# Performance work log

Measured on AMD Instinct MI355X. Metric: run time of the kernel, lower is better.

Reference implementation:

```python
import jax, jax.numpy as jnp
import numpy as np

B, L, K, E, D, H = 16, 512, 48, 128, 384, 128

def _gelu(x):
    return jax.nn.gelu(x, approximate=False)  # torch nn.GELU default is erf-based

def setup_inputs() -> dict:
    key = jax.random.key(0)
    ks = jax.random.split(key, 16)
    def randn(k, shape, scale=1.0):
        return jax.random.normal(k, shape, dtype=jnp.float32) * scale
    inp = {
        "h_V": randn(ks[0], (B, L, D)),
        "h_E": randn(ks[1], (B, L, K, E)),
        "mask": jnp.ones((B, L), dtype=jnp.float32),
        "fw1": randn(ks[2], (E, D), 1.0 / np.sqrt(E)),
        "fb1": randn(ks[3], (D,), 0.02),
        "fw2": randn(ks[4], (D, D), 1.0 / np.sqrt(D)),
        "fb2": randn(ks[5], (D,), 0.02),
        "hw1": randn(ks[6], (D, H), 1.0 / np.sqrt(D)),
        "hb1": randn(ks[7], (H,), 0.02),
        "hw2": randn(ks[8], (H, H // 2), 1.0 / np.sqrt(H)),
        "hb2": randn(ks[9], (H // 2,), 0.02),
        "hw3": randn(ks[10], (H // 2, 1), 1.0 / np.sqrt(H // 2)),
        "hb3": randn(ks[11], (1,), 0.02),
        "E_idx": jax.random.randint(ks[12], (B, L, K), 0, L),
    }
    return inp

def reference(h_V, h_E, mask, fw1, fb1, fw2, fb2, hw1, hb1, hw2, hb2, hw3, hb3, E_idx):
    # CFConv: edge-conditioned filters [B,L,K,D]
    W = _gelu(_gelu(h_E @ fw1 + fb1) @ fw2 + fb2)
    # gather_nodes: x_j[b,l,k,:] = h_V[b, E_idx[b,l,k], :]
    x_j = jax.vmap(lambda x, idx: x[idx])(h_V, E_idx)  # [B,L,K,D]
    h = jnp.sum(x_j * W, axis=2)  # weighted sum over neighbors -> [B,L,D]
    # mlp_head (dropout = identity at inference)
    h = _gelu(h @ hw1 + hb1)
    h = _gelu(h @ hw2 + hb2)
    dG = (h @ hw3 + hb3)[..., 0]  # [B,L]
    valid_length = jnp.clip(jnp.sum(mask, axis=1), 1.0, None)  # [B]
    return jnp.sum(dG * mask, axis=1) / jnp.sqrt(valid_length)  # [B]
```

## Files before the change

kernel.cpp:

```cpp
#include <hip/hip_runtime.h>
#include <hip/hip_bf16.h>
#include <math.h>

#define NB 16
#define NL 512
#define NK 48
#define NE 128
#define ND 384
#define NH 128

typedef __attribute__((ext_vector_type(8))) short short8;
typedef __attribute__((ext_vector_type(4))) float f32x4;

__device__ __forceinline__ float gelu_fast(float x) {
    float t = x * fmaf(x * x, -0.1029437f, -2.3022087f);
    float e = __builtin_amdgcn_exp2f(t);
    return x * __builtin_amdgcn_rcpf(1.0f + e);
}

__device__ __forceinline__ unsigned short f2bf(float x) {
    union { float f; unsigned u; } v; v.f = x;
    unsigned r = v.u + 0x7fffu + ((v.u >> 16) & 1u);
    return (unsigned short)(r >> 16);
}

__device__ __forceinline__ unsigned short f2bf_rhu(float x) {
    union { float f; unsigned u; } v; v.f = x;
    return (unsigned short)((v.u + 0x8000u) >> 16);
}

__device__ __forceinline__ unsigned pk_bf16(float a, float b) {
    union { float f; unsigned u; } ua, ub; ua.f = a; ub.f = b;
    return __builtin_amdgcn_perm(ua.u + 0x8000u, ub.u + 0x8000u, 0x07060302u);
}

__global__ void pack_weights(const float* __restrict__ fw1,
                             const float* __restrict__ fw2,
                             const float* __restrict__ hw1,
                             const float* __restrict__ hw2,
                             unsigned short* __restrict__ fw1p,
                             unsigned short* __restrict__ fw2p,
                             unsigned short* __restrict__ hw1p,
                             unsigned short* __restrict__ hw2p) {
    int tid = blockIdx.x * 256 + threadIdx.x;
    if (tid < NE * ND) {
        int k = tid / ND, n = tid % ND;
        int dst = (((k >> 5) * 24 + (n >> 4)) * 64 + ((k >> 3) & 3) * 16 + (n & 15)) * 8 + (k & 7);
        fw1p[dst] = f2bf(fw1[tid]);
    } else if (tid < NE * ND + ND * ND) {
        int i = tid - NE * ND;
        int k = i / ND, n = i % ND;
        int dst = (((k >> 5) * 24 + (n >> 4)) * 64 + ((k >> 3) & 3) * 16 + (n & 15)) * 8 + (k & 7);
        fw2p[dst] = f2bf(fw2[i]);
    } else if (tid < NE * ND + ND * ND + ND * NH) {
        int i = tid - (NE * ND + ND * ND);
        int k = i / NH, n = i % NH;
        int dst = (((k >> 5) * 8 + (n >> 4)) * 64 + ((k >> 3) & 3) * 16 + (n & 15)) * 8 + (k & 7);
        hw1p[dst] = f2bf(hw1[i]);
    } else if (tid < NE * ND + ND * ND + ND * NH + NH * (NH / 2)) {
        int i = tid - (NE * ND + ND * ND + ND * NH);
        int k = i / (NH / 2), n = i % (NH / 2);
        int dst = (((k >> 5) * 4 + (n >> 4)) * 64 + ((k >> 3) & 3) * 16 + (n & 15)) * 8 + (k & 7);
        hw2p[dst] = f2bf(hw2[i]);
    }
}

__global__ __launch_bounds__(256, 3) void cfconv_kernel(
    const float* __restrict__ h_V, const float* __restrict__ h_E,
    const float* __restrict__ fb1, const float* __restrict__ fb2,
    const unsigned short* __restrict__ fw1p,
    const unsigned short* __restrict__ fw2p,
    const int* __restrict__ E_idx, unsigned short* __restrict__ hbufB)
{
    __shared__ unsigned short Ea[48 * 136];
    __shared__ unsigned short T[48 * 392];
    __shared__ int rowoff_s[48];

    const int t = threadIdx.x;
    const int wave = t >> 6, lane = t & 63;
    const int quad = lane >> 4, l16 = lane & 15;
    const int bl = blockIdx.x;
    const int wn0 = wave * 96;

    if (t < 48)
        rowoff_s[t] = ((bl >> 9) * NL + E_idx[bl * NK + t]) * ND;

    {
        const float4* src = (const float4*)(h_E + (size_t)bl * (NK * NE));
        #pragma unroll
        for (int i = 0; i < 6; i++) {
            int v = i * 256 + t;
            float4 d = src[v];
            int r = v >> 5;
            int c = (v & 31) * 4;
            uint2 u;
            u.x = pk_bf16(d.y, d.x);
            u.y = pk_bf16(d.w, d.z);
            *(uint2*)&Ea[r * 136 + c] = u;
        }
    }
    __syncthreads();

    f32x4 acc[18];

    #pragma unroll
    for (int i = 0; i < 18; i++) acc[i] = (f32x4){0.f, 0.f, 0.f, 0.f};

    #pragma unroll
    for (int kt = 0; kt < 4; kt++) {
        short8 aw[6], be[3];
        #pragma unroll
        for (int mt = 0; mt < 6; mt++)
            aw[mt] = *(const short8*)(fw1p + (size_t)((kt * 24 + (wn0 >> 4) + mt) * 64 + lane) * 8);
        #pragma unroll
        for (int nt = 0; nt < 3; nt++)
            be[nt] = *(const short8*)&Ea[(nt * 16 + l16) * 136 + kt * 32 + quad * 8];
        #pragma unroll
        for (int mt = 0; mt < 6; mt++)
            #pragma unroll
            for (int nt = 0; nt < 3; nt++)
                acc[mt * 3 + nt] = __builtin_amdgcn_mfma_f32_16x16x32_bf16(
                    aw[mt], be[nt], acc[mt * 3 + nt], 0, 0, 0);
    }

    #pragma unroll
    for (int mt = 0; mt < 6; mt++) {
        float4 b1v = *(const float4*)&fb1[wn0 + mt * 16 + quad * 4];
        #pragma unroll
        for (int nt = 0; nt < 3; nt++) {
            f32x4 a = acc[mt * 3 + nt];
            float v0 = gelu_fast(a[0] + b1v.x);
            float v1 = gelu_fast(a[1] + b1v.y);
            float v2 = gelu_fast(a[2] + b1v.z);
            float v3 = gelu_fast(a[3] + b1v.w);
            uint2 u;
            u.x = pk_bf16(v1, v0);
            u.y = pk_bf16(v3, v2);
            *(uint2*)&T[(nt * 16 + l16) * 392 + wn0 + mt * 16 + quad * 4] = u;
        }
    }
    __syncthreads();

    #pragma unroll
    for (int i = 0; i < 18; i++) acc[i] = (f32x4){0.f, 0.f, 0.f, 0.f};

    {
        short8 b0[6], b1[6], af[3];
        #define LOADB(kt, bf)                                                            \
            _Pragma("unroll")                                                            \
            for (int nt = 0; nt < 6; nt++)                                               \
                bf[nt] = *(const short8*)(fw2p +                                         \
                    (size_t)(((kt) * 24 + (wn0 >> 4) + nt) * 64 + lane) * 8);
        #define LOADA(kt)                                                                \
            _Pragma("unroll")                                                            \
            for (int mt = 0; mt < 3; mt++)                                               \
                af[mt] = *(const short8*)&T[(mt * 16 + l16) * 392 + (kt) * 32 + quad * 8];
        #define MFMAS(bf)                                                                \
            _Pragma("unroll")                                                            \
            for (int mt = 0; mt < 3; mt++)                                               \
                _Pragma("unroll")                                                        \
                for (int nt = 0; nt < 6; nt++)                                           \
                    acc[nt * 3 + mt] = __builtin_amdgcn_mfma_f32_16x16x32_bf16(          \
                        af[mt], bf[nt], acc[nt * 3 + mt], 0, 0, 0);

        LOADB(0, b0);
        for (int kt = 0; kt < 10; kt += 2) {
            LOADB(kt + 1, b1);
            LOADA(kt);
            MFMAS(b0);
            LOADB(kt + 2, b0);
            LOADA(kt + 1);
            MFMAS(b1);
        }
        LOADB(11, b1);
        LOADA(10);
        MFMAS(b0);
        LOADA(11);
        MFMAS(b1);
        #undef LOADB
        #undef LOADA
        #undef MFMAS
    }

    float b2v[6];
    #pragma unroll
    for (int nt = 0; nt < 6; nt++) b2v[nt] = fb2[wn0 + nt * 16 + l16];

    float s[6] = {0.f, 0.f, 0.f, 0.f, 0.f, 0.f};
    #pragma unroll
    for (int mt = 0; mt < 3; mt++) {
        const int rb = mt * 16 + quad * 4;
        const float* p0 = h_V + rowoff_s[rb + 0] + wn0 + l16;
        const float* p1 = h_V + rowoff_s[rb + 1] + wn0 + l16;
        const float* p2 = h_V + rowoff_s[rb + 2] + wn0 + l16;
        const float* p3 = h_V + rowoff_s[rb + 3] + wn0 + l16;
        float xv[6][4];
        #pragma unroll
        for (int nt = 0; nt < 6; nt++) {
            xv[nt][0] = p0[nt * 16];
            xv[nt][1] = p1[nt * 16];
            xv[nt][2] = p2[nt * 16];
            xv[nt][3] = p3[nt * 16];
        }
        #pragma unroll
        for (int nt = 0; nt < 6; nt++)
            #pragma unroll
            for (int r = 0; r < 4; r++)
                s[nt] = fmaf(gelu_fast(acc[nt * 3 + mt][r] + b2v[nt]), xv[nt][r], s[nt]);
    }
    #pragma unroll
    for (int nt = 0; nt < 6; nt++) {
        float v = s[nt];
        v += __shfl_xor(v, 16, 64);
        v += __shfl_xor(v, 32, 64);
        if (lane < 16)
            hbufB[(size_t)bl * ND + wn0 + nt * 16 + lane] = f2bf(v);
    }
}

__global__ __launch_bounds__(64) void head_kernel(
    const unsigned short* __restrict__ hbufB,
    const unsigned short* __restrict__ hw1p, const float* __restrict__ hb1,
    const unsigned short* __restrict__ hw2p, const float* __restrict__ hb2,
    const float* __restrict__ hw3, const float* __restrict__ hb3,
    const float* __restrict__ mask, float* __restrict__ dGpart)
{
    __shared__ unsigned short T1[16 * 136];
    const int lane = threadIdx.x;
    const int quad = lane >> 4, l16 = lane & 15;
    const int row0 = blockIdx.x * 16;

    f32x4 acc1[8];
    #pragma unroll
    for (int nt = 0; nt < 8; nt++) acc1[nt] = (f32x4){0.f, 0.f, 0.f, 0.f};

    for (int kt = 0; kt < 12; kt++) {
        short8 a = *(const short8*)(hbufB + (size_t)(row0 + l16) * ND + kt * 32 + quad * 8);
        #pragma unroll
        for (int nt = 0; nt < 8; nt++) {
            short8 b = *(const short8*)(hw1p + (size_t)((kt * 8 + nt) * 64 + lane) * 8);
            acc1[nt] = __builtin_amdgcn_mfma_f32_16x16x32_bf16(a, b, acc1[nt], 0, 0, 0);
        }
    }

    #pragma unroll
    for (int nt = 0; nt < 8; nt++) {
        int col = nt * 16 + l16;
        float b1 = hb1[col];
        #pragma unroll
        for (int r = 0; r < 4; r++)
            T1[(quad * 4 + r) * 136 + col] = f2bf_rhu(gelu_fast(acc1[nt][r] + b1));
    }
    __syncthreads();

    f32x4 acc2[4];
    #pragma unroll
    for (int nt = 0; nt < 4; nt++) acc2[nt] = (f32x4){0.f, 0.f, 0.f, 0.f};

    #pragma unroll
    for (int kt = 0; kt < 4; kt++) {
        short8 a = *(const short8*)&T1[l16 * 136 + kt * 32 + quad * 8];
        #pragma unroll
        for (int nt = 0; nt < 4; nt++) {
            short8 b = *(const short8*)(hw2p + (size_t)((kt * 4 + nt) * 64 + lane) * 8);
            acc2[nt] = __builtin_amdgcn_mfma_f32_16x16x32_bf16(a, b, acc2[nt], 0, 0, 0);
        }
    }

    float w3[4], b2[4];
    #pragma unroll
    for (int nt = 0; nt < 4; nt++) { w3[nt] = hw3[nt * 16 + l16]; b2[nt] = hb2[nt * 16 + l16]; }

    float dsum = 0.f;
    const float hb3v = hb3[0];
    #pragma unroll
    for (int r = 0; r < 4; r++) {
        float pr = 0.f;
        #pragma unroll
        for (int nt = 0; nt < 4; nt++)
            pr = fmaf(gelu_fast(acc2[nt][r] + b2[nt]), w3[nt], pr);
        pr += __shfl_xor(pr, 1, 64);
        pr += __shfl_xor(pr, 2, 64);
        pr += __shfl_xor(pr, 4, 64);
        pr += __shfl_xor(pr, 8, 64);
        if (l16 == 0) {
            int grow = row0 + quad * 4 + r;
            dsum = fmaf(pr + hb3v, mask[grow], dsum);
        }
    }
    dsum += __shfl_xor(dsum, 16, 64);
    dsum += __shfl_xor(dsum, 32, 64);
    if (lane == 0) dGpart[blockIdx.x] = dsum;
}

__global__ void finalize_kernel(const float* __restrict__ dGpart,
                                const float* __restrict__ mask,
                                float* __restrict__ out) {
    int t = threadIdx.x;
    int b = t >> 4, j = t & 15;
    float ms = 0.f;
    for (int l = j; l < NL; l += 16) ms += mask[b * NL + l];
    float dg = dGpart[b * 32 + j] + dGpart[b * 32 + 16 + j];
    #pragma unroll
    for (int d = 1; d < 16; d <<= 1) {
        ms += __shfl_xor(ms, d, 64);
        dg += __shfl_xor(dg, d, 64);
    }
    if (j == 0) {
        ms = fmaxf(ms, 1.0f);
        out[b] = dg / sqrtf(ms);
    }
}

extern "C" void kernel_launch(void* const* d_in, const int* in_sizes, int n_in,
                              void* d_out, int out_size, void* d_ws, size_t ws_size,
                              hipStream_t stream) {
    const float* h_V  = (const float*)d_in[0];
    const float* h_E  = (const float*)d_in[1];
    const float* mask = (const float*)d_in[2];
    const float* fw1  = (const float*)d_in[3];
    const float* fb1  = (const float*)d_in[4];
    const float* fw2  = (const float*)d_in[5];
    const float* fb2  = (const float*)d_in[6];
    const float* hw1  = (const float*)d_in[7];
    const float* hb1  = (const float*)d_in[8];
    const float* hw2  = (const float*)d_in[9];
    const float* hb2  = (const float*)d_in[10];
    const float* hw3  = (const float*)d_in[11];
    const float* hb3  = (const float*)d_in[12];
    const int*   E_idx = (const int*)d_in[13];
    float* out = (float*)d_out;

    char* ws = (char*)d_ws;
    unsigned short* fw1p = (unsigned short*)ws;
    unsigned short* fw2p = (unsigned short*)(ws + 98304);
    unsigned short* hw1p = (unsigned short*)(ws + 393216);
    unsigned short* hw2p = (unsigned short*)(ws + 491520);
    float* dGpart = (float*)(ws + 507904);
    unsigned short* hbufB = (unsigned short*)(ws + 512000);

    pack_weights<<<992, 256, 0, stream>>>(fw1, fw2, hw1, hw2, fw1p, fw2p, hw1p, hw2p);
    cfconv_kernel<<<NB * NL, 256, 0, stream>>>(h_V, h_E, fb1, fb2, fw1p, fw2p, E_idx, hbufB);
    head_kernel<<<(NB * NL) / 16, 64, 0, stream>>>(hbufB, hw1p, hb1, hw2p, hb2, hw3, hb3, mask, dGpart);
    finalize_kernel<<<1, 256, 0, stream>>>(dGpart, mask, out);
}
```

Measured before the change: 466.9 us.

## Alias cfconv LDS buffers, raise occupancy, split head across two waves, vectorize packing

The cfconv kernel now shares one LDS buffer between the edge-feature tile and the intermediate filter tile, with an extra barrier before the overwrite. Launch bounds are raised to target four blocks per CU, which cuts LDS per block to allow more resident blocks. The head kernel splits its output columns across two waves and writes twice as many partials, and finalize sums four partials per row. Weight packing writes 8 bf16 values per thread as one vector store. The tighter occupancy target may force register spills in the main kernel.

```diff
diff --git a/kernel.cpp b/kernel.cpp
--- a/kernel.cpp
+++ b/kernel.cpp
@@ -43,38 +43,33 @@
                              unsigned short* __restrict__ hw1p,
                              unsigned short* __restrict__ hw2p) {
     int tid = blockIdx.x * 256 + threadIdx.x;
-    if (tid < NE * ND) {
-        int k = tid / ND, n = tid % ND;
-        int dst = (((k >> 5) * 24 + (n >> 4)) * 64 + ((k >> 3) & 3) * 16 + (n & 15)) * 8 + (k & 7);
-        fw1p[dst] = f2bf(fw1[tid]);
-    } else if (tid < NE * ND + ND * ND) {
-        int i = tid - NE * ND;
-        int k = i / ND, n = i % ND;
-        int dst = (((k >> 5) * 24 + (n >> 4)) * 64 + ((k >> 3) & 3) * 16 + (n & 15)) * 8 + (k & 7);
-        fw2p[dst] = f2bf(fw2[i]);
-    } else if (tid < NE * ND + ND * ND + ND * NH) {
-        int i = tid - (NE * ND + ND * ND);
-        int k = i / NH, n = i % NH;
-        int dst = (((k >> 5) * 8 + (n >> 4)) * 64 + ((k >> 3) & 3) * 16 + (n & 15)) * 8 + (k & 7);
-        hw1p[dst] = f2bf(hw1[i]);
-    } else if (tid < NE * ND + ND * ND + ND * NH + NH * (NH / 2)) {
-        int i = tid - (NE * ND + ND * ND + ND * NH);
-        int k = i / (NH / 2), n = i % (NH / 2);
-        int dst = (((k >> 5) * 4 + (n >> 4)) * 64 + ((k >> 3) & 3) * 16 + (n & 15)) * 8 + (k & 7);
-        hw2p[dst] = f2bf(hw2[i]);
-    }
-}
-
-__global__ __launch_bounds__(256, 3) void cfconv_kernel(
+    const float* src; unsigned short* dst; int N, NT, idx;
+    if (tid < 6144)        { src = fw1; dst = fw1p; N = ND;     NT = 24; idx = tid; }
+    else if (tid < 24576)  { src = fw2; dst = fw2p; N = ND;     NT = 24; idx = tid - 6144; }
+    else if (tid < 30720)  { src = hw1; dst = hw1p; N = NH;     NT = 8;  idx = tid - 24576; }
+    else                   { src = hw2; dst = hw2p; N = NH / 2; NT = 4;  idx = tid - 30720; }
+    int kg = idx / N;
+    int n  = idx - kg * N;
+    int k0 = kg * 8;
+    int base = (((k0 >> 5) * NT + (n >> 4)) * 64 + ((k0 >> 3) & 3) * 16 + (n & 15)) * 8;
+    short8 v;
+    #pragma unroll
+    for (int j = 0; j < 8; j++)
+        v[j] = (short)f2bf(src[(size_t)(k0 + j) * N + n]);
+    *(short8*)(dst + base) = v;
+}
+
+__global__ __launch_bounds__(256, 4) void cfconv_kernel(
     const float* __restrict__ h_V, const float* __restrict__ h_E,
     const float* __restrict__ fb1, const float* __restrict__ fb2,
     const unsigned short* __restrict__ fw1p,
     const unsigned short* __restrict__ fw2p,
     const int* __restrict__ E_idx, unsigned short* __restrict__ hbufB)
 {
-    __shared__ unsigned short Ea[48 * 136];
-    __shared__ unsigned short T[48 * 392];
+    __shared__ unsigned short SH[48 * 392];
     __shared__ int rowoff_s[48];
+    unsigned short* const Ea = SH;
+    unsigned short* const T  = SH;
 
     const int t = threadIdx.x;
     const int wave = t >> 6, lane = t & 63;
@@ -122,6 +117,8 @@
                 acc[mt * 3 + nt] = __builtin_amdgcn_mfma_f32_16x16x32_bf16(
                     aw[mt], be[nt], acc[mt * 3 + nt], 0, 0, 0);
     }
+
+    __syncthreads();
 
     #pragma unroll
     for (int mt = 0; mt < 6; mt++) {
@@ -218,7 +215,7 @@
     }
 }
 
-__global__ __launch_bounds__(64) void head_kernel(
+__global__ __launch_bounds__(128) void head_kernel(
     const unsigned short* __restrict__ hbufB,
     const unsigned short* __restrict__ hw1p, const float* __restrict__ hb1,
     const unsigned short* __restrict__ hw2p, const float* __restrict__ hb2,
@@ -226,26 +223,28 @@
     const float* __restrict__ mask, float* __restrict__ dGpart)
 {
     __shared__ unsigned short T1[16 * 136];
-    const int lane = threadIdx.x;
+    const int t = threadIdx.x;
+    const int w = t >> 6;
+    const int lane = t & 63;
     const int quad = lane >> 4, l16 = lane & 15;
     const int row0 = blockIdx.x * 16;
 
-    f32x4 acc1[8];
-    #pragma unroll
-    for (int nt = 0; nt < 8; nt++) acc1[nt] = (f32x4){0.f, 0.f, 0.f, 0.f};
+    f32x4 acc1[4];
+    #pragma unroll
+    for (int nt = 0; nt < 4; nt++) acc1[nt] = (f32x4){0.f, 0.f, 0.f, 0.f};
 
     for (int kt = 0; kt < 12; kt++) {
         short8 a = *(const short8*)(hbufB + (size_t)(row0 + l16) * ND + kt * 32 + quad * 8);
         #pragma unroll
-        for (int nt = 0; nt < 8; nt++) {
-            short8 b = *(const short8*)(hw1p + (size_t)((kt * 8 + nt) * 64 + lane) * 8);
+        for (int nt = 0; nt < 4; nt++) {
+            short8 b = *(const short8*)(hw1p + (size_t)((kt * 8 + w * 4 + nt) * 64 + lane) * 8);
             acc1[nt] = __builtin_amdgcn_mfma_f32_16x16x32_bf16(a, b, acc1[nt], 0, 0, 0);
         }
     }
 
     #pragma unroll
-    for (int nt = 0; nt < 8; nt++) {
-        int col = nt * 16 + l16;
+    for (int nt = 0; nt < 4; nt++) {
+        int col = (w * 4 + nt) * 16 + l16;
         float b1 = hb1[col];
         #pragma unroll
         for (int r = 0; r < 4; r++)
@@ -253,31 +252,35 @@
     }
     __syncthreads();
 
-    f32x4 acc2[4];
-    #pragma unroll
-    for (int nt = 0; nt < 4; nt++) acc2[nt] = (f32x4){0.f, 0.f, 0.f, 0.f};
+    f32x4 acc2[2];
+    #pragma unroll
+    for (int nt = 0; nt < 2; nt++) acc2[nt] = (f32x4){0.f, 0.f, 0.f, 0.f};
 
     #pragma unroll
     for (int kt = 0; kt < 4; kt++) {
         short8 a = *(const short8*)&T1[l16 * 136 + kt * 32 + quad * 8];
         #pragma unroll
-        for (int nt = 0; nt < 4; nt++) {
-            short8 b = *(const short8*)(hw2p + (size_t)((kt * 4 + nt) * 64 + lane) * 8);
+        for (int nt = 0; nt < 2; nt++) {
+            short8 b = *(const short8*)(hw2p + (size_t)((kt * 4 + w * 2 + nt) * 64 + lane) * 8);
             acc2[nt] = __builtin_amdgcn_mfma_f32_16x16x32_bf16(a, b, acc2[nt], 0, 0, 0);
         }
     }
 
-    float w3[4], b2[4];
-    #pragma unroll
-    for (int nt = 0; nt < 4; nt++) { w3[nt] = hw3[nt * 16 + l16]; b2[nt] = hb2[nt * 16 + l16]; }
+    float w3[2], b2[2];
+    #pragma unroll
+    for (int nt = 0; nt < 2; nt++) {
+        int col = (w * 2 + nt) * 16 + l16;
+        w3[nt] = hw3[col];
+        b2[nt] = hb2[col];
+    }
 
     float dsum = 0.f;
-    const float hb3v = hb3[0];
+    const float hb3h = 0.5f * hb3[0];
     #pragma unroll
     for (int r = 0; r < 4; r++) {
         float pr = 0.f;
         #pragma unroll
-        for (int nt = 0; nt < 4; nt++)
+        for (int nt = 0; nt < 2; nt++)
             pr = fmaf(gelu_fast(acc2[nt][r] + b2[nt]), w3[nt], pr);
         pr += __shfl_xor(pr, 1, 64);
         pr += __shfl_xor(pr, 2, 64);
@@ -285,12 +288,12 @@
         pr += __shfl_xor(pr, 8, 64);
         if (l16 == 0) {
             int grow = row0 + quad * 4 + r;
-            dsum = fmaf(pr + hb3v, mask[grow], dsum);
+            dsum = fmaf(pr + hb3h, mask[grow], dsum);
         }
     }
     dsum += __shfl_xor(dsum, 16, 64);
     dsum += __shfl_xor(dsum, 32, 64);
-    if (lane == 0) dGpart[blockIdx.x] = dsum;
+    if (lane == 0) dGpart[blockIdx.x * 2 + w] = dsum;
 }
 
 __global__ void finalize_kernel(const float* __restrict__ dGpart,
@@ -300,7 +303,8 @@
     int b = t >> 4, j = t & 15;
     float ms = 0.f;
     for (int l = j; l < NL; l += 16) ms += mask[b * NL + l];
-    float dg = dGpart[b * 32 + j] + dGpart[b * 32 + 16 + j];
+    float dg = dGpart[b * 64 + j] + dGpart[b * 64 + 16 + j]
+             + dGpart[b * 64 + 32 + j] + dGpart[b * 64 + 48 + j];
     #pragma unroll
     for (int d = 1; d < 16; d <<= 1) {
         ms += __shfl_xor(ms, d, 64);
@@ -339,8 +343,8 @@
     float* dGpart = (float*)(ws + 507904);
     unsigned short* hbufB = (unsigned short*)(ws + 512000);
 
-    pack_weights<<<992, 256, 0, stream>>>(fw1, fw2, hw1, hw2, fw1p, fw2p, hw1p, hw2p);
+    pack_weights<<<124, 256, 0, stream>>>(fw1, fw2, hw1, hw2, fw1p, fw2p, hw1p, hw2p);
     cfconv_kernel<<<NB * NL, 256, 0, stream>>>(h_V, h_E, fb1, fb2, fw1p, fw2p, E_idx, hbufB);
-    head_kernel<<<(NB * NL) / 16, 64, 0, stream>>>(hbufB, hw1p, hb1, hw2p, hb2, hw3, hb3, mask, dGpart);
+    head_kernel<<<(NB * NL) / 16, 128, 0, stream>>>(hbufB, hw1p, hb1, hw2p, hb2, hw3, hb3, mask, dGpart);
     finalize_kernel<<<1, 256, 0, stream>>>(dGpart, mask, out);
 }
```

Measured after the change: 504.8 us. +8.1%, slower.
